# Kernel optimization log

Measured on AMD Instinct MI355X. Metric: run time of the kernel, lower is better.

The kernel has to match this reference:

```python
import jax, jax.numpy as jnp
import numpy as np

N, E, H, DE = 50000, 800000, 128, 16

def silu(x):
    return x * jax.nn.sigmoid(x)

def setup_inputs() -> dict:
    key = jax.random.key(0)
    ks = jax.random.split(key, 24)
    def W(k, i, o, s=0.02):
        return (jax.random.normal(k, (i, o), jnp.float32) * s)
    inp = {
        'h': jax.random.normal(ks[0], (N, H), jnp.float32),
        'coord': jax.random.normal(ks[1], (N, 3), jnp.float32),
        'edge_index': jax.random.randint(ks[2], (2, E), 0, N),
        'edge_attr': jax.random.normal(ks[3], (E, DE), jnp.float32),
        # mes_mlp: Linear(2H+1+DE -> H), SiLU, Linear(H -> H), SiLU
        'mes_w1': W(ks[4], 2 * H + 1 + DE, H), 'mes_b1': jnp.zeros((H,), jnp.float32),
        'mes_w2': W(ks[5], H, H),              'mes_b2': jnp.zeros((H,), jnp.float32),
        # edge_mlp: Linear(H+1+DE -> H), SiLU, Linear(H -> H)
        'edge_w1': W(ks[6], H + 1 + DE, H),    'edge_b1': jnp.zeros((H,), jnp.float32),
        'edge_w2': W(ks[7], H, H),             'edge_b2': jnp.zeros((H,), jnp.float32),
        # node_mlp: Linear(H+H -> H), SiLU, Linear(H -> H)
        'node_w1': W(ks[8], 2 * H, H),         'node_b1': jnp.zeros((H,), jnp.float32),
        'node_w2': W(ks[9], H, H),             'node_b2': jnp.zeros((H,), jnp.float32),
        # coord_mlp: Linear(H -> H), SiLU, Linear(H -> 1, no bias, xavier gain 0.001)
        'coord_w1': W(ks[10], H, H),           'coord_b1': jnp.zeros((H,), jnp.float32),
        'coord_w2': W(ks[11], H, 1, s=0.001),
    }
    return inp

def reference(h, coord, edge_index, edge_attr,
              mes_w1, mes_b1, mes_w2, mes_b2,
              edge_w1, edge_b1, edge_w2, edge_b2,
              node_w1, node_b1, node_w2, node_b2,
              coord_w1, coord_b1, coord_w2):
    row, col = edge_index[0], edge_index[1]
    n = h.shape[0]
    # coord2radial
    coord_diff = coord[row] - coord[col]                        # [E,3]
    radial = jnp.sum(coord_diff ** 2, axis=1, keepdims=True)    # [E,1]
    norm = jnp.sqrt(radial + 1e-8)
    coord_diff = coord_diff / (norm + 1.0)
    # mes_model
    mes_in = jnp.concatenate([h[row], h[col], radial, edge_attr], axis=1)
    edge_feat = silu(silu(mes_in @ mes_w1 + mes_b1) @ mes_w2 + mes_b2)  # [E,H]
    # coord_model (agg='sum', no tanh)
    trans = coord_diff * (silu(edge_feat @ coord_w1 + coord_b1) @ coord_w2)  # [E,3]
    coord = coord + jax.ops.segment_sum(trans, col, num_segments=n)
    # node_model (recurrent)
    agg = jax.ops.segment_sum(edge_feat, col, num_segments=n)   # [N,H]
    node_in = jnp.concatenate([h, agg], axis=1)
    h = h + (silu(node_in @ node_w1 + node_b1) @ node_w2 + node_b2)
    # edge_model
    edge_in = jnp.concatenate([edge_feat, radial, edge_attr], axis=1)
    edge_out = silu(edge_in @ edge_w1 + edge_b1) @ edge_w2 + edge_b2
    return (h, coord, edge_out)
```

## Files before the change

kernel.cpp:

```cpp
#include <hip/hip_runtime.h>
#include <cstdint>
#include <cstddef>

typedef float f32x4 __attribute__((ext_vector_type(4)));
typedef __bf16 bf16x8 __attribute__((ext_vector_type(8)));
typedef __bf16 bf16x4 __attribute__((ext_vector_type(4)));
typedef __bf16 bf16x2 __attribute__((ext_vector_type(2)));
typedef unsigned short u16;

#define Hdim 128
#define DEdim 16
#define TP 40

__device__ __forceinline__ float bf2f(uint32_t lo16){
  return __builtin_bit_cast(float, lo16 << 16);
}
__device__ __forceinline__ float bfhi(uint32_t v){
  return __builtin_bit_cast(float, v & 0xffff0000u);
}
__device__ __forceinline__ float silu_f(float x){
  return x / (1.0f + __expf(-x));
}
__device__ __forceinline__ uint32_t addbf2(uint32_t a, uint32_t b){
  float lo = bf2f(a & 0xffffu) + bf2f(b & 0xffffu);
  float hi = bfhi(a) + bfhi(b);
  bf16x2 p; p[0] = (__bf16)lo; p[1] = (__bf16)hi;
  return __builtin_bit_cast(uint32_t, p);
}
__device__ __forceinline__ uint2 pack4(f32x4 v){
  bf16x4 p;
  #pragma unroll
  for (int i=0;i<4;++i) p[i] = (__bf16)v[i];
  return __builtin_bit_cast(uint2, p);
}
__device__ __forceinline__ uint2 silu_pack4(const f32x4& v, f32x4* sout=nullptr){
  f32x4 s;
  #pragma unroll
  for (int i=0;i<4;++i) s[i] = silu_f(v[i]);
  if (sout) *sout = s;
  return pack4(s);
}

template<int KC>
__device__ __forceinline__ void gemm_sw(
    const u16* A, int apitch,
    const u16* __restrict__ Wt, int kpad, int woff,
    int wv, int cidx, int hi, f32x4 (&acc)[4][2])
{
  const u16* w0p = Wt + (size_t)((wv*2+0)*16 + cidx)*kpad + woff + hi*8;
  const u16* w1p = Wt + (size_t)((wv*2+1)*16 + cidx)*kpad + woff + hi*8;
  const u16* ap  = A + (size_t)cidx*apitch + hi*8;
  #pragma unroll
  for (int kc=0; kc<KC; ++kc){
    bf16x8 w0 = *(const bf16x8*)(w0p + kc*32);
    bf16x8 w1 = *(const bf16x8*)(w1p + kc*32);
    #pragma unroll
    for (int et=0; et<4; ++et){
      bf16x8 a = *(const bf16x8*)(ap + et*16*apitch + kc*32);
      acc[et][0] = __builtin_amdgcn_mfma_f32_16x16x32_bf16(w0, a, acc[et][0], 0,0,0);
      acc[et][1] = __builtin_amdgcn_mfma_f32_16x16x32_bf16(w1, a, acc[et][1], 0,0,0);
    }
  }
}

__device__ __forceinline__ void acc_bias(const float* __restrict__ bias,
                                         int wv, int hi, f32x4 (&acc)[4][2])
{
  f32x4 b0 = *(const f32x4*)(bias + (wv*2+0)*16 + hi*4);
  f32x4 b1 = *(const f32x4*)(bias + (wv*2+1)*16 + hi*4);
  #pragma unroll
  for (int et=0;et<4;++et){ acc[et][0]=b0; acc[et][1]=b1; }
}

template<int SP>
__device__ __forceinline__ void write_silu_S(u16* S, f32x4 (&acc)[4][2],
                                             int wv, int cidx, int hi)
{
  #pragma unroll
  for (int et=0; et<4; ++et){
    const int e = et*16 + cidx;
    #pragma unroll
    for (int j=0;j<2;++j){
      const int f0 = (wv*2+j)*16 + hi*4;
      *(uint2*)(S + (size_t)e*SP + f0) = silu_pack4(acc[et][j]);
    }
  }
}

template<bool PROJ, bool GATHER>
__global__ __launch_bounds__(256, PROJ?4:3) void egcl_edge(
    const float* __restrict__ h, const float* __restrict__ coord,
    const int* __restrict__ ei, const float* __restrict__ ea,
    const u16* __restrict__ proj, const int* __restrict__ pos,
    const float* __restrict__ mes_b1, const float* __restrict__ mes_b2,
    const float* __restrict__ edge_b1, const float* __restrict__ edge_b2,
    const float* __restrict__ coord_b1, const float* __restrict__ coord_w2,
    const u16* __restrict__ w_mes1t, const u16* __restrict__ w_mes2t,
    const u16* __restrict__ w_coord1t, const u16* __restrict__ w_edge1t,
    const u16* __restrict__ w_edge2t,
    float* __restrict__ agg, u16* __restrict__ featb,
    float* __restrict__ out_coord, float* __restrict__ out_edge, int E)
{
  constexpr int SP = PROJ ? 136 : 264;
  __shared__ u16 S[64*SP];
  __shared__ u16 T[64*TP];
  __shared__ float cds[64*4];
  __shared__ float tvs[4][64];
  __shared__ int cnode[64];
  __shared__ int epos[64];

  const int tid  = threadIdx.x;
  const int lane = tid & 63;
  const int wv   = tid >> 6;
  const int e0   = blockIdx.x * 64;
  const int cidx = lane & 15;
  const int hi   = lane >> 4;

  {
    const int le   = wv*16 + (lane>>2);
    const int part = lane & 3;
    int eg = e0 + le; if (eg >= E) eg = E-1;
    const int rn = ei[eg], cn = ei[E + eg];
    if constexpr (PROJ){
      const uint4* pr = (const uint4*)(proj + (size_t)rn*256 + part*32);
      const uint4* pc = (const uint4*)(proj + (size_t)cn*256 + 128 + part*32);
      u16* dst = S + (size_t)le*SP + part*32;
      #pragma unroll
      for (int q=0;q<4;++q){
        uint4 a = pr[q], b = pc[q], o;
        o.x = addbf2(a.x, b.x); o.y = addbf2(a.y, b.y);
        o.z = addbf2(a.z, b.z); o.w = addbf2(a.w, b.w);
        *(uint4*)(dst + q*8) = o;
      }
    } else {
      const float* src = ((part<2) ? h + (size_t)rn*Hdim : h + (size_t)cn*Hdim) + (part&1)*64;
      u16* dst = S + (size_t)le*SP + part*64;
      #pragma unroll
      for (int q=0;q<16;++q){
        float4 v = ((const float4*)src)[q];
        bf16x4 o = {(__bf16)v.x,(__bf16)v.y,(__bf16)v.z,(__bf16)v.w};
        *(bf16x4*)(dst + q*4) = o;
      }
    }
    if (part == 0){
      cnode[le] = cn;
      if constexpr (GATHER) epos[le] = pos[eg];
      const float dx = coord[(size_t)rn*3+0] - coord[(size_t)cn*3+0];
      const float dy = coord[(size_t)rn*3+1] - coord[(size_t)cn*3+1];
      const float dz = coord[(size_t)rn*3+2] - coord[(size_t)cn*3+2];
      const float radial = dx*dx + dy*dy + dz*dz;
      const float inv = 1.0f/(sqrtf(radial + 1e-8f) + 1.0f);
      cds[le*4+0]=dx*inv; cds[le*4+1]=dy*inv; cds[le*4+2]=dz*inv; cds[le*4+3]=radial;
      u16* tp = T + le*TP;
      const float4* eap = (const float4*)(ea + (size_t)eg*DEdim);
      #pragma unroll
      for (int q=0;q<4;++q){
        float4 v = eap[q];
        bf16x4 o = {(__bf16)v.x,(__bf16)v.y,(__bf16)v.z,(__bf16)v.w};
        *(bf16x4*)(tp + q*4) = o;
      }
      bf16x4 z = {(__bf16)0.f,(__bf16)0.f,(__bf16)0.f,(__bf16)0.f};
      *(bf16x4*)(tp+16) = z; *(bf16x4*)(tp+20) = z;
      *(bf16x4*)(tp+24) = z; *(bf16x4*)(tp+28) = z;
      *(__bf16*)(tp+16) = (__bf16)radial;
    }
    ((float*)tvs)[tid] = 0.f;
  }
  __syncthreads();

  f32x4 acc[4][2];

  acc_bias(mes_b1, wv, hi, acc);
  if constexpr (PROJ){
    #pragma unroll
    for (int et=0;et<4;++et){
      const int e = et*16 + cidx;
      #pragma unroll
      for (int j=0;j<2;++j){
        const int f0 = (wv*2+j)*16 + hi*4;
        ushort4 sv = *(const ushort4*)(S + (size_t)e*SP + f0);
        acc[et][j][0] += bf2f(sv.x); acc[et][j][1] += bf2f(sv.y);
        acc[et][j][2] += bf2f(sv.z); acc[et][j][3] += bf2f(sv.w);
      }
    }
    gemm_sw<1>(T, TP, w_mes1t, 288, 256, wv, cidx, hi, acc);
  } else {
    gemm_sw<8>(S, SP, w_mes1t, 288, 0,   wv, cidx, hi, acc);
    gemm_sw<1>(T, TP, w_mes1t, 288, 256, wv, cidx, hi, acc);
    __syncthreads();
  }
  write_silu_S<SP>(S, acc, wv, cidx, hi);
  __syncthreads();

  acc_bias(mes_b2, wv, hi, acc);
  gemm_sw<4>(S, SP, w_mes2t, 128, 0, wv, cidx, hi, acc);
  uint2 ps[4][2];
  #pragma unroll
  for (int et=0;et<4;++et)
    #pragma unroll
    for (int j=0;j<2;++j){
      f32x4 sv;
      ps[et][j] = silu_pack4(acc[et][j], &sv);
      if constexpr (!GATHER){
        const int e = et*16 + cidx;
        if (e0 + e < E){
          const int f0 = (wv*2+j)*16 + hi*4;
          #pragma unroll
          for (int i=0;i<4;++i)
            atomicAdd(agg + (size_t)cnode[e]*Hdim + f0 + i, sv[i]);
        }
      }
    }
  __syncthreads();
  #pragma unroll
  for (int et=0;et<4;++et)
    #pragma unroll
    for (int j=0;j<2;++j)
      *(uint2*)(S + (size_t)(et*16+cidx)*SP + (wv*2+j)*16 + hi*4) = ps[et][j];
  __syncthreads();

  if constexpr (GATHER){
    const int row = tid >> 2, seg = tid & 3;
    if (e0 + row < E){
      const int4* s = (const int4*)(S + (size_t)row*SP + seg*32);
      int4* d = (int4*)(featb + (size_t)epos[row]*Hdim + seg*32);
      d[0]=s[0]; d[1]=s[1]; d[2]=s[2]; d[3]=s[3];
    }
  }

  acc_bias(coord_b1, wv, hi, acc);
  gemm_sw<4>(S, SP, w_coord1t, 128, 0, wv, cidx, hi, acc);
  {
    f32x4 cw0 = *(const f32x4*)(coord_w2 + (wv*2+0)*16 + hi*4);
    f32x4 cw1 = *(const f32x4*)(coord_w2 + (wv*2+1)*16 + hi*4);
    #pragma unroll
    for (int et=0;et<4;++et){
      float p = 0.f;
      #pragma unroll
      for (int i=0;i<4;++i)
        p += silu_f(acc[et][0][i])*cw0[i] + silu_f(acc[et][1][i])*cw1[i];
      p += __shfl_xor(p, 16);
      p += __shfl_xor(p, 32);
      if (hi == 0) tvs[wv][et*16+cidx] = p;
    }
  }

  acc_bias(edge_b1, wv, hi, acc);
  gemm_sw<4>(S, SP, w_edge1t, 160, 0,   wv, cidx, hi, acc);
  gemm_sw<1>(T, TP, w_edge1t, 160, 128, wv, cidx, hi, acc);
  #pragma unroll
  for (int et=0;et<4;++et)
    #pragma unroll
    for (int j=0;j<2;++j)
      ps[et][j] = silu_pack4(acc[et][j]);
  __syncthreads();
  if (tid < 192){
    const int le = tid/3, d = tid - le*3;
    if (e0 + le < E){
      const float t4 = tvs[0][le]+tvs[1][le]+tvs[2][le]+tvs[3][le];
      atomicAdd(out_coord + (size_t)cnode[le]*3 + d, cds[le*4+d]*t4);
    }
  }
  #pragma unroll
  for (int et=0;et<4;++et)
    #pragma unroll
    for (int j=0;j<2;++j)
      *(uint2*)(S + (size_t)(et*16+cidx)*SP + (wv*2+j)*16 + hi*4) = ps[et][j];
  __syncthreads();

  acc_bias(edge_b2, wv, hi, acc);
  gemm_sw<4>(S, SP, w_edge2t, 128, 0, wv, cidx, hi, acc);
  #pragma unroll
  for (int et=0;et<4;++et){
    const int e = e0 + et*16 + cidx;
    if (e < E){
      #pragma unroll
      for (int j=0;j<2;++j)
        *(f32x4*)(out_edge + (size_t)e*Hdim + (wv*2+j)*16 + hi*4) = acc[et][j];
    }
  }
}

__global__ __launch_bounds__(256, 4) void egcl_proj(
    const float* __restrict__ h, const u16* __restrict__ w_mes1t,
    u16* __restrict__ proj, int N)
{
  __shared__ u16 S[64*136];
  const int tid=threadIdx.x, lane=tid&63, wv=tid>>6, cidx=lane&15, hi=lane>>4;
  const int r0 = blockIdx.x*64, half = blockIdx.y;
  {
    const int le = tid>>2, part = tid&3;
    int g = r0 + le; if (g >= N) g = N-1;
    const float* src = h + (size_t)g*Hdim + part*32;
    u16* dst = S + (size_t)le*136 + part*32;
    #pragma unroll
    for (int q=0;q<8;++q){
      float4 v = ((const float4*)src)[q];
      bf16x4 o = {(__bf16)v.x,(__bf16)v.y,(__bf16)v.z,(__bf16)v.w};
      *(bf16x4*)(dst + q*4) = o;
    }
  }
  __syncthreads();
  f32x4 acc[4][2];
  #pragma unroll
  for (int et=0;et<4;++et){ acc[et][0]=(f32x4){0,0,0,0}; acc[et][1]=(f32x4){0,0,0,0}; }
  gemm_sw<4>(S, 136, w_mes1t, 288, half*128, wv, cidx, hi, acc);
  #pragma unroll
  for (int et=0;et<4;++et){
    const int g = r0 + et*16 + cidx;
    if (g < N){
      #pragma unroll
      for (int j=0;j<2;++j)
        *(uint2*)(proj + (size_t)g*256 + half*128 + (wv*2+j)*16 + hi*4) = pack4(acc[et][j]);
    }
  }
}

template<bool GATHER>
__global__ __launch_bounds__(256, 4) void egcl_node(
    const float* __restrict__ h, const float* __restrict__ agg,
    const int* __restrict__ offs, const int* __restrict__ deg,
    const u16* __restrict__ featb,
    const float* __restrict__ node_b1, const float* __restrict__ node_b2,
    const u16* __restrict__ w_node1t, const u16* __restrict__ w_node2t,
    float* __restrict__ out_h, int N)
{
  __shared__ u16 Ab[64*264];
  const int tid=threadIdx.x, lane=tid&63, wv=tid>>6, cidx=lane&15, hi=lane>>4;
  const int r0 = blockIdx.x*64;
  {
    const int le = tid>>2, part = tid&3;
    int g = r0 + le; if (g >= N) g = N-1;
    const float* src = h + (size_t)g*Hdim + part*32;
    u16* dst = Ab + (size_t)le*264 + part*32;
    #pragma unroll
    for (int q=0;q<8;++q){
      float4 v = ((const float4*)src)[q];
      bf16x4 o = {(__bf16)v.x,(__bf16)v.y,(__bf16)v.z,(__bf16)v.w};
      *(bf16x4*)(dst + q*4) = o;
    }
  }
  if constexpr (GATHER){
    const int le = tid>>2, part = tid&3;
    const int g = r0 + le;
    float a[32];
    #pragma unroll
    for (int q=0;q<32;++q) a[q]=0.f;
    if (g < N){
      const int s = offs[g], dg = deg[g];
      const u16* base = featb + (size_t)s*Hdim + part*32;
      #pragma unroll 2
      for (int r=0;r<dg;++r){
        const uint4* rp = (const uint4*)(base + (size_t)r*Hdim);
        #pragma unroll
        for (int q=0;q<4;++q){
          uint4 w = rp[q];
          a[q*8+0] += bf2f(w.x & 0xffffu); a[q*8+1] += bfhi(w.x);
          a[q*8+2] += bf2f(w.y & 0xffffu); a[q*8+3] += bfhi(w.y);
          a[q*8+4] += bf2f(w.z & 0xffffu); a[q*8+5] += bfhi(w.z);
          a[q*8+6] += bf2f(w.w & 0xffffu); a[q*8+7] += bfhi(w.w);
        }
      }
    }
    u16* dst = Ab + (size_t)le*264 + 128 + part*32;
    #pragma unroll
    for (int q=0;q<8;++q){
      bf16x4 o = {(__bf16)a[q*4+0],(__bf16)a[q*4+1],(__bf16)a[q*4+2],(__bf16)a[q*4+3]};
      *(bf16x4*)(dst + q*4) = o;
    }
  } else {
    const int le = tid>>2, part = tid&3;
    int g = r0 + le; if (g >= N) g = N-1;
    const float* src = agg + (size_t)g*Hdim + part*32;
    u16* dst = Ab + (size_t)le*264 + 128 + part*32;
    #pragma unroll
    for (int q=0;q<8;++q){
      float4 v = ((const float4*)src)[q];
      bf16x4 o = {(__bf16)v.x,(__bf16)v.y,(__bf16)v.z,(__bf16)v.w};
      *(bf16x4*)(dst + q*4) = o;
    }
  }
  __syncthreads();

  f32x4 acc[4][2];
  acc_bias(node_b1, wv, hi, acc);
  gemm_sw<8>(Ab, 264, w_node1t, 256, 0, wv, cidx, hi, acc);
  __syncthreads();
  write_silu_S<264>(Ab, acc, wv, cidx, hi);
  __syncthreads();
  acc_bias(node_b2, wv, hi, acc);
  gemm_sw<4>(Ab, 264, w_node2t, 128, 0, wv, cidx, hi, acc);
  #pragma unroll
  for (int et=0;et<4;++et){
    const int g = r0 + et*16 + cidx;
    if (g < N){
      #pragma unroll
      for (int j=0;j<2;++j){
        const int f0 = (wv*2+j)*16 + hi*4;
        f32x4 hv = *(const f32x4*)(h + (size_t)g*Hdim + f0);
        hv += acc[et][j];
        *(f32x4*)(out_h + (size_t)g*Hdim + f0) = hv;
      }
    }
  }
}

__global__ void egcl_init(const float* __restrict__ coord, float* __restrict__ out_coord,
                          int nc, float* __restrict__ zf, int nzf,
                          int* __restrict__ zi, int nzi)
{
  const int i = blockIdx.x*256 + threadIdx.x;
  if (i < nc) out_coord[i] = coord[i];
  if (zf && i < nzf) zf[i] = 0.f;
  if (zi && i < nzi) zi[i] = 0;
}

__global__ void egcl_wconv7(
    const float* s0, const float* s1, const float* s2, const float* s3,
    const float* s4, const float* s5, const float* s6, u16* __restrict__ dst)
{
  static const int kpads[7]  = {288,128,128,160,128,256,128};
  static const int Ks[7]     = {273,128,128,145,128,256,128};
  static const int modes[7]  = {1,0,0,2,0,0,0};
  const int gi = blockIdx.x*256 + threadIdx.x;
  int w = 0, off = 0, boff = 0;
  #pragma unroll
  for (int t=0;t<7;++t){
    const int sz = 128*kpads[t];
    if (gi >= off && gi < off + sz){ w = t; boff = off; }
    off += sz;
  }
  if (gi >= off) return;
  const float* srcs[7] = {s0,s1,s2,s3,s4,s5,s6};
  const int li = gi - boff;
  const int kpad = kpads[w], K = Ks[w], mode = modes[w];
  const int c = li / kpad, k = li - c*kpad;
  int ks;
  if (mode==1)      ks = (k<256) ? k : (k<272 ? k+1 : (k==272 ? 256 : -1));
  else if (mode==2) ks = (k<128) ? k : (k<144 ? k+1 : (k==144 ? 128 : -1));
  else              ks = (k<K) ? k : -1;
  const float v = (ks>=0) ? srcs[w][(size_t)ks*128 + c] : 0.f;
  *(__bf16*)(dst + gi) = (__bf16)v;
}

__global__ void k_hist(const int* __restrict__ ei, int* __restrict__ hist, int E){
  const int i = blockIdx.x*256 + threadIdx.x;
  if (i < E) atomicAdd(&hist[ei[E + i]], 1);
}
__global__ void k_scan1(const int* __restrict__ hist, int* __restrict__ partial, int N){
  __shared__ int s[256];
  const int t = threadIdx.x, i = blockIdx.x*256 + t;
  s[t] = (i < N) ? hist[i] : 0;
  __syncthreads();
  for (int o=128; o>0; o>>=1){ if (t < o) s[t] += s[t+o]; __syncthreads(); }
  if (t == 0) partial[blockIdx.x] = s[0];
}
__global__ void k_scan2(int* __restrict__ partial, int G){
  if (blockIdx.x == 0 && threadIdx.x == 0){
    int run = 0;
    for (int i=0;i<G;++i){ const int v = partial[i]; partial[i] = run; run += v; }
  }
}
__global__ void k_scan3(const int* __restrict__ hist, const int* __restrict__ partial,
                        int* __restrict__ offs, int* __restrict__ cursor, int N){
  __shared__ int s[256];
  const int t = threadIdx.x, i = blockIdx.x*256 + t;
  const int v = (i < N) ? hist[i] : 0;
  s[t] = v;
  __syncthreads();
  for (int o=1; o<256; o<<=1){
    int x = (t >= o) ? s[t-o] : 0;
    __syncthreads();
    s[t] += x;
    __syncthreads();
  }
  const int ex = s[t] - v + partial[blockIdx.x];
  if (i < N){ offs[i] = ex; cursor[i] = ex; }
}
__global__ void k_scatter(const int* __restrict__ ei, int* __restrict__ cursor,
                          int* __restrict__ pos, int E){
  const int i = blockIdx.x*256 + threadIdx.x;
  if (i < E){
    const int c = ei[E + i];
    pos[i] = atomicAdd(&cursor[c], 1);
  }
}

extern "C" void kernel_launch(void* const* d_in, const int* in_sizes, int n_in,
                              void* d_out, int out_size, void* d_ws, size_t ws_size,
                              hipStream_t stream)
{
  const float* h       = (const float*)d_in[0];
  const float* coord   = (const float*)d_in[1];
  const int*   ei      = (const int*)d_in[2];
  const float* ea      = (const float*)d_in[3];
  const float* mes_w1  = (const float*)d_in[4];
  const float* mes_b1  = (const float*)d_in[5];
  const float* mes_w2  = (const float*)d_in[6];
  const float* mes_b2  = (const float*)d_in[7];
  const float* edge_w1 = (const float*)d_in[8];
  const float* edge_b1 = (const float*)d_in[9];
  const float* edge_w2 = (const float*)d_in[10];
  const float* edge_b2 = (const float*)d_in[11];
  const float* node_w1 = (const float*)d_in[12];
  const float* node_b1 = (const float*)d_in[13];
  const float* node_w2 = (const float*)d_in[14];
  const float* node_b2 = (const float*)d_in[15];
  const float* coord_w1= (const float*)d_in[16];
  const float* coord_b1= (const float*)d_in[17];
  const float* coord_w2= (const float*)d_in[18];

  const int N = in_sizes[0] / Hdim;
  const int E = in_sizes[2] / 2;
  const int G1 = (N + 255) / 256;

  char* ws = (char*)d_ws;
  const size_t wtot = (size_t)(288+128+128+160+128+256+128)*128;
  u16* wbase     = (u16*)ws;
  u16* w_mes1t   = wbase;
  u16* w_mes2t   = w_mes1t  + 128*288;
  u16* w_coord1t = w_mes2t  + 128*128;
  u16* w_edge1t  = w_coord1t+ 128*128;
  u16* w_edge2t  = w_edge1t + 128*160;
  u16* w_node1t  = w_edge2t + 128*128;
  u16* w_node2t  = w_node1t + 128*256;

  auto al = [](size_t x){ return (x + 255) & ~(size_t)255; };
  const size_t base   = al(wtot*2);
  const size_t o_feat = base;
  const size_t o_hist = o_feat + al((size_t)E*Hdim*2);
  const size_t o_offs = o_hist + al((size_t)N*4);
  const size_t o_cur  = o_offs + al((size_t)N*4);
  const size_t o_part = o_cur  + al((size_t)N*4);
  const size_t o_pos  = o_part + al((size_t)G1*4);
  const size_t gather_end = o_pos + al((size_t)E*4);
  const size_t o_proj = gather_end;
  const size_t proj_end = o_proj + (size_t)N*256*2;
  const bool gather = (ws_size >= gather_end);
  const bool proj   = (ws_size >= proj_end);

  float* out_h     = (float*)d_out;
  float* out_coord = out_h + (size_t)N*Hdim;
  float* out_edge  = out_coord + (size_t)N*3;

  const int wblocks = (int)((wtot + 255)/256);
  egcl_wconv7<<<wblocks, 256, 0, stream>>>(mes_w1, mes_w2, coord_w1, edge_w1,
                                           edge_w2, node_w1, node_w2, wbase);

  if (gather){
    u16* featb  = (u16*)(ws + o_feat);
    int* hist   = (int*)(ws + o_hist);
    int* offs   = (int*)(ws + o_offs);
    int* cursor = (int*)(ws + o_cur);
    int* partial= (int*)(ws + o_part);
    int* pos    = (int*)(ws + o_pos);
    u16* projp  = (u16*)(ws + o_proj);

    egcl_init<<<(N*3+255)/256, 256, 0, stream>>>(coord, out_coord, N*3, nullptr, 0, hist, N);
    k_hist<<<(E+255)/256, 256, 0, stream>>>(ei, hist, E);
    k_scan1<<<G1, 256, 0, stream>>>(hist, partial, N);
    k_scan2<<<1, 64, 0, stream>>>(partial, G1);
    k_scan3<<<G1, 256, 0, stream>>>(hist, partial, offs, cursor, N);
    k_scatter<<<(E+255)/256, 256, 0, stream>>>(ei, cursor, pos, E);

    if (proj){
      dim3 pg((N+63)/64, 2);
      egcl_proj<<<pg, 256, 0, stream>>>(h, w_mes1t, projp, N);
      egcl_edge<true,true><<<(E+63)/64, 256, 0, stream>>>(h, coord, ei, ea, projp, pos,
          mes_b1, mes_b2, edge_b1, edge_b2, coord_b1, coord_w2,
          w_mes1t, w_mes2t, w_coord1t, w_edge1t, w_edge2t,
          nullptr, featb, out_coord, out_edge, E);
    } else {
      egcl_edge<false,true><<<(E+63)/64, 256, 0, stream>>>(h, coord, ei, ea, nullptr, pos,
          mes_b1, mes_b2, edge_b1, edge_b2, coord_b1, coord_w2,
          w_mes1t, w_mes2t, w_coord1t, w_edge1t, w_edge2t,
          nullptr, featb, out_coord, out_edge, E);
    }
    egcl_node<true><<<(N+63)/64, 256, 0, stream>>>(h, nullptr, offs, hist, featb,
        node_b1, node_b2, w_node1t, w_node2t, out_h, N);
  } else {
    float* agg = (float*)(ws + base);
    egcl_init<<<(N*Hdim+255)/256, 256, 0, stream>>>(coord, out_coord, N*3, agg, N*Hdim, nullptr, 0);
    egcl_edge<false,false><<<(E+63)/64, 256, 0, stream>>>(h, coord, ei, ea, nullptr, nullptr,
        mes_b1, mes_b2, edge_b1, edge_b2, coord_b1, coord_w2,
        w_mes1t, w_mes2t, w_coord1t, w_edge1t, w_edge2t,
        agg, nullptr, out_coord, out_edge, E);
    egcl_node<false><<<(N+63)/64, 256, 0, stream>>>(h, agg, nullptr, nullptr, nullptr,
        node_b1, node_b2, w_node1t, w_node2t, out_h, N);
  }
}
```

Before: 636.8 us.

## Give each wave its own 16-edge slab and drop block-wide barriers

Work is repartitioned so that each wave owns 16 edges (or nodes) and computes all 128 output features for them, rather than all four waves sharing 64 edges split by feature. Every wave now reads and writes only its own slice of shared memory, so all __syncthreads calls and the cross-wave reduction through tvs are removed. Launch bounds for the non-projection path are also raised to 4 blocks. The cost is that each wave now reads the whole weight matrix from global or L1 for only 16 edges, so weight traffic per edge goes up fourfold, and the 8 accumulators plus the preloaded A fragments increase register pressure.

```diff
diff --git a/kernel.cpp b/kernel.cpp
--- a/kernel.cpp
+++ b/kernel.cpp
@@ -42,6 +42,38 @@
 }
 
 template<int KC>
+__device__ __forceinline__ void gemm_w(
+    const u16* Sw, int sp,
+    const u16* __restrict__ Wt, int kpad, int woff,
+    int cidx, int hi, f32x4 (&acc)[8])
+{
+  bf16x8 a[KC];
+  const u16* ap = Sw + (size_t)cidx*sp + hi*8;
+  #pragma unroll
+  for (int kc=0; kc<KC; ++kc) a[kc] = *(const bf16x8*)(ap + kc*32);
+  #pragma unroll
+  for (int j=0;j<8;++j){
+    const u16* wp = Wt + (size_t)(j*16+cidx)*kpad + woff + hi*8;
+    #pragma unroll
+    for (int kc=0; kc<KC; ++kc){
+      bf16x8 w = *(const bf16x8*)(wp + kc*32);
+      acc[j] = __builtin_amdgcn_mfma_f32_16x16x32_bf16(w, a[kc], acc[j], 0,0,0);
+    }
+  }
+}
+
+__device__ __forceinline__ void bias8(const float* __restrict__ b, int hi, f32x4 (&acc)[8]){
+  #pragma unroll
+  for (int j=0;j<8;++j) acc[j] = *(const f32x4*)(b + j*16 + hi*4);
+}
+
+__device__ __forceinline__ void silu_store8(u16* Sw, int sp, int cidx, int hi, f32x4 (&acc)[8]){
+  #pragma unroll
+  for (int j=0;j<8;++j)
+    *(uint2*)(Sw + (size_t)cidx*sp + j*16 + hi*4) = silu_pack4(acc[j]);
+}
+
+template<int KC>
 __device__ __forceinline__ void gemm_sw(
     const u16* A, int apitch,
     const u16* __restrict__ Wt, int kpad, int woff,
@@ -63,32 +95,8 @@
   }
 }
 
-__device__ __forceinline__ void acc_bias(const float* __restrict__ bias,
-                                         int wv, int hi, f32x4 (&acc)[4][2])
-{
-  f32x4 b0 = *(const f32x4*)(bias + (wv*2+0)*16 + hi*4);
-  f32x4 b1 = *(const f32x4*)(bias + (wv*2+1)*16 + hi*4);
-  #pragma unroll
-  for (int et=0;et<4;++et){ acc[et][0]=b0; acc[et][1]=b1; }
-}
-
-template<int SP>
-__device__ __forceinline__ void write_silu_S(u16* S, f32x4 (&acc)[4][2],
-                                             int wv, int cidx, int hi)
-{
-  #pragma unroll
-  for (int et=0; et<4; ++et){
-    const int e = et*16 + cidx;
-    #pragma unroll
-    for (int j=0;j<2;++j){
-      const int f0 = (wv*2+j)*16 + hi*4;
-      *(uint2*)(S + (size_t)e*SP + f0) = silu_pack4(acc[et][j]);
-    }
-  }
-}
-
 template<bool PROJ, bool GATHER>
-__global__ __launch_bounds__(256, PROJ?4:3) void egcl_edge(
+__global__ __launch_bounds__(256, 4) void egcl_edge(
     const float* __restrict__ h, const float* __restrict__ coord,
     const int* __restrict__ ei, const float* __restrict__ ea,
     const u16* __restrict__ proj, const int* __restrict__ pos,
@@ -105,26 +113,28 @@
   __shared__ u16 S[64*SP];
   __shared__ u16 T[64*TP];
   __shared__ float cds[64*4];
-  __shared__ float tvs[4][64];
+  __shared__ float tvs[64];
   __shared__ int cnode[64];
   __shared__ int epos[64];
 
   const int tid  = threadIdx.x;
   const int lane = tid & 63;
   const int wv   = tid >> 6;
-  const int e0   = blockIdx.x * 64;
   const int cidx = lane & 15;
   const int hi   = lane >> 4;
+  const int e0   = blockIdx.x*64 + wv*16;
+  u16* Sw = S + (size_t)wv*16*SP;
+  u16* Tw = T + (size_t)wv*16*TP;
 
   {
-    const int le   = wv*16 + (lane>>2);
+    const int le   = lane >> 2;
     const int part = lane & 3;
     int eg = e0 + le; if (eg >= E) eg = E-1;
     const int rn = ei[eg], cn = ei[E + eg];
     if constexpr (PROJ){
       const uint4* pr = (const uint4*)(proj + (size_t)rn*256 + part*32);
       const uint4* pc = (const uint4*)(proj + (size_t)cn*256 + 128 + part*32);
-      u16* dst = S + (size_t)le*SP + part*32;
+      u16* dst = Sw + (size_t)le*SP + part*32;
       #pragma unroll
       for (int q=0;q<4;++q){
         uint4 a = pr[q], b = pc[q], o;
@@ -134,7 +144,7 @@
       }
     } else {
       const float* src = ((part<2) ? h + (size_t)rn*Hdim : h + (size_t)cn*Hdim) + (part&1)*64;
-      u16* dst = S + (size_t)le*SP + part*64;
+      u16* dst = Sw + (size_t)le*SP + part*64;
       #pragma unroll
       for (int q=0;q<16;++q){
         float4 v = ((const float4*)src)[q];
@@ -143,15 +153,16 @@
       }
     }
     if (part == 0){
-      cnode[le] = cn;
-      if constexpr (GATHER) epos[le] = pos[eg];
+      const int gle = wv*16 + le;
+      cnode[gle] = cn;
+      if constexpr (GATHER) epos[gle] = pos[eg];
       const float dx = coord[(size_t)rn*3+0] - coord[(size_t)cn*3+0];
       const float dy = coord[(size_t)rn*3+1] - coord[(size_t)cn*3+1];
       const float dz = coord[(size_t)rn*3+2] - coord[(size_t)cn*3+2];
       const float radial = dx*dx + dy*dy + dz*dz;
       const float inv = 1.0f/(sqrtf(radial + 1e-8f) + 1.0f);
-      cds[le*4+0]=dx*inv; cds[le*4+1]=dy*inv; cds[le*4+2]=dz*inv; cds[le*4+3]=radial;
-      u16* tp = T + le*TP;
+      cds[gle*4+0]=dx*inv; cds[gle*4+1]=dy*inv; cds[gle*4+2]=dz*inv; cds[gle*4+3]=radial;
+      u16* tp = Tw + le*TP;
       const float4* eap = (const float4*)(ea + (size_t)eg*DEdim);
       #pragma unroll
       for (int q=0;q<4;++q){
@@ -164,119 +175,84 @@
       *(bf16x4*)(tp+24) = z; *(bf16x4*)(tp+28) = z;
       *(__bf16*)(tp+16) = (__bf16)radial;
     }
-    ((float*)tvs)[tid] = 0.f;
-  }
-  __syncthreads();
-
-  f32x4 acc[4][2];
-
-  acc_bias(mes_b1, wv, hi, acc);
+  }
+
+  f32x4 acc[8];
+
+  bias8(mes_b1, hi, acc);
   if constexpr (PROJ){
     #pragma unroll
-    for (int et=0;et<4;++et){
-      const int e = et*16 + cidx;
-      #pragma unroll
-      for (int j=0;j<2;++j){
-        const int f0 = (wv*2+j)*16 + hi*4;
-        ushort4 sv = *(const ushort4*)(S + (size_t)e*SP + f0);
-        acc[et][j][0] += bf2f(sv.x); acc[et][j][1] += bf2f(sv.y);
-        acc[et][j][2] += bf2f(sv.z); acc[et][j][3] += bf2f(sv.w);
+    for (int j=0;j<8;++j){
+      ushort4 sv = *(const ushort4*)(Sw + (size_t)cidx*SP + j*16 + hi*4);
+      acc[j][0] += bf2f(sv.x); acc[j][1] += bf2f(sv.y);
+      acc[j][2] += bf2f(sv.z); acc[j][3] += bf2f(sv.w);
+    }
+  } else {
+    gemm_w<4>(Sw,       SP, w_mes1t, 288, 0,   cidx, hi, acc);
+    gemm_w<4>(Sw + 128, SP, w_mes1t, 288, 128, cidx, hi, acc);
+  }
+  gemm_w<1>(Tw, TP, w_mes1t, 288, 256, cidx, hi, acc);
+  silu_store8(Sw, SP, cidx, hi, acc);
+
+  bias8(mes_b2, hi, acc);
+  gemm_w<4>(Sw, SP, w_mes2t, 128, 0, cidx, hi, acc);
+  #pragma unroll
+  for (int j=0;j<8;++j){
+    f32x4 sv;
+    uint2 pk = silu_pack4(acc[j], &sv);
+    *(uint2*)(Sw + (size_t)cidx*SP + j*16 + hi*4) = pk;
+    if constexpr (!GATHER){
+      if (e0 + cidx < E){
+        #pragma unroll
+        for (int i=0;i<4;++i)
+          atomicAdd(agg + (size_t)cnode[wv*16+cidx]*Hdim + j*16 + hi*4 + i, sv[i]);
       }
     }
-    gemm_sw<1>(T, TP, w_mes1t, 288, 256, wv, cidx, hi, acc);
-  } else {
-    gemm_sw<8>(S, SP, w_mes1t, 288, 0,   wv, cidx, hi, acc);
-    gemm_sw<1>(T, TP, w_mes1t, 288, 256, wv, cidx, hi, acc);
-    __syncthreads();
-  }
-  write_silu_S<SP>(S, acc, wv, cidx, hi);
-  __syncthreads();
-
-  acc_bias(mes_b2, wv, hi, acc);
-  gemm_sw<4>(S, SP, w_mes2t, 128, 0, wv, cidx, hi, acc);
-  uint2 ps[4][2];
-  #pragma unroll
-  for (int et=0;et<4;++et)
-    #pragma unroll
-    for (int j=0;j<2;++j){
-      f32x4 sv;
-      ps[et][j] = silu_pack4(acc[et][j], &sv);
-      if constexpr (!GATHER){
-        const int e = et*16 + cidx;
-        if (e0 + e < E){
-          const int f0 = (wv*2+j)*16 + hi*4;
-          #pragma unroll
-          for (int i=0;i<4;++i)
-            atomicAdd(agg + (size_t)cnode[e]*Hdim + f0 + i, sv[i]);
-        }
-      }
-    }
-  __syncthreads();
-  #pragma unroll
-  for (int et=0;et<4;++et)
-    #pragma unroll
-    for (int j=0;j<2;++j)
-      *(uint2*)(S + (size_t)(et*16+cidx)*SP + (wv*2+j)*16 + hi*4) = ps[et][j];
-  __syncthreads();
+  }
 
   if constexpr (GATHER){
-    const int row = tid >> 2, seg = tid & 3;
-    if (e0 + row < E){
-      const int4* s = (const int4*)(S + (size_t)row*SP + seg*32);
-      int4* d = (int4*)(featb + (size_t)epos[row]*Hdim + seg*32);
+    const int le = lane >> 2, seg = lane & 3;
+    if (e0 + le < E){
+      const int4* s = (const int4*)(Sw + (size_t)le*SP + seg*32);
+      int4* d = (int4*)(featb + (size_t)epos[wv*16+le]*Hdim + seg*32);
       d[0]=s[0]; d[1]=s[1]; d[2]=s[2]; d[3]=s[3];
     }
   }
 
-  acc_bias(coord_b1, wv, hi, acc);
-  gemm_sw<4>(S, SP, w_coord1t, 128, 0, wv, cidx, hi, acc);
+  bias8(coord_b1, hi, acc);
+  gemm_w<4>(Sw, SP, w_coord1t, 128, 0, cidx, hi, acc);
   {
-    f32x4 cw0 = *(const f32x4*)(coord_w2 + (wv*2+0)*16 + hi*4);
-    f32x4 cw1 = *(const f32x4*)(coord_w2 + (wv*2+1)*16 + hi*4);
-    #pragma unroll
-    for (int et=0;et<4;++et){
-      float p = 0.f;
-      #pragma unroll
-      for (int i=0;i<4;++i)
-        p += silu_f(acc[et][0][i])*cw0[i] + silu_f(acc[et][1][i])*cw1[i];
-      p += __shfl_xor(p, 16);
-      p += __shfl_xor(p, 32);
-      if (hi == 0) tvs[wv][et*16+cidx] = p;
-    }
-  }
-
-  acc_bias(edge_b1, wv, hi, acc);
-  gemm_sw<4>(S, SP, w_edge1t, 160, 0,   wv, cidx, hi, acc);
-  gemm_sw<1>(T, TP, w_edge1t, 160, 128, wv, cidx, hi, acc);
-  #pragma unroll
-  for (int et=0;et<4;++et)
-    #pragma unroll
-    for (int j=0;j<2;++j)
-      ps[et][j] = silu_pack4(acc[et][j]);
-  __syncthreads();
-  if (tid < 192){
-    const int le = tid/3, d = tid - le*3;
-    if (e0 + le < E){
-      const float t4 = tvs[0][le]+tvs[1][le]+tvs[2][le]+tvs[3][le];
-      atomicAdd(out_coord + (size_t)cnode[le]*3 + d, cds[le*4+d]*t4);
-    }
-  }
-  #pragma unroll
-  for (int et=0;et<4;++et)
-    #pragma unroll
-    for (int j=0;j<2;++j)
-      *(uint2*)(S + (size_t)(et*16+cidx)*SP + (wv*2+j)*16 + hi*4) = ps[et][j];
-  __syncthreads();
-
-  acc_bias(edge_b2, wv, hi, acc);
-  gemm_sw<4>(S, SP, w_edge2t, 128, 0, wv, cidx, hi, acc);
-  #pragma unroll
-  for (int et=0;et<4;++et){
-    const int e = e0 + et*16 + cidx;
+    float p = 0.f;
+    #pragma unroll
+    for (int j=0;j<8;++j){
+      f32x4 cw = *(const f32x4*)(coord_w2 + j*16 + hi*4);
+      #pragma unroll
+      for (int i=0;i<4;++i) p += silu_f(acc[j][i])*cw[i];
+    }
+    p += __shfl_xor(p, 16);
+    p += __shfl_xor(p, 32);
+    if (hi == 0) tvs[wv*16 + cidx] = p;
+  }
+  if (lane < 48){
+    const int le = lane/3, d = lane - le*3;
+    if (e0 + le < E)
+      atomicAdd(out_coord + (size_t)cnode[wv*16+le]*3 + d,
+                cds[(wv*16+le)*4+d]*tvs[wv*16+le]);
+  }
+
+  bias8(edge_b1, hi, acc);
+  gemm_w<4>(Sw, SP, w_edge1t, 160, 0,   cidx, hi, acc);
+  gemm_w<1>(Tw, TP, w_edge1t, 160, 128, cidx, hi, acc);
+  silu_store8(Sw, SP, cidx, hi, acc);
+
+  bias8(edge_b2, hi, acc);
+  gemm_w<4>(Sw, SP, w_edge2t, 128, 0, cidx, hi, acc);
+  {
+    const int e = e0 + cidx;
     if (e < E){
       #pragma unroll
-      for (int j=0;j<2;++j)
-        *(f32x4*)(out_edge + (size_t)e*Hdim + (wv*2+j)*16 + hi*4) = acc[et][j];
+      for (int j=0;j<8;++j)
+        *(f32x4*)(out_edge + (size_t)e*Hdim + j*16 + hi*4) = acc[j];
     }
   }
 }
@@ -327,12 +303,14 @@
 {
   __shared__ u16 Ab[64*264];
   const int tid=threadIdx.x, lane=tid&63, wv=tid>>6, cidx=lane&15, hi=lane>>4;
-  const int r0 = blockIdx.x*64;
+  const int r0 = blockIdx.x*64 + wv*16;
+  u16* Aw = Ab + (size_t)wv*16*264;
+
   {
-    const int le = tid>>2, part = tid&3;
+    const int le = lane>>2, part = lane&3;
     int g = r0 + le; if (g >= N) g = N-1;
     const float* src = h + (size_t)g*Hdim + part*32;
-    u16* dst = Ab + (size_t)le*264 + part*32;
+    u16* dst = Aw + (size_t)le*264 + part*32;
     #pragma unroll
     for (int q=0;q<8;++q){
       float4 v = ((const float4*)src)[q];
@@ -341,7 +319,7 @@
     }
   }
   if constexpr (GATHER){
-    const int le = tid>>2, part = tid&3;
+    const int le = lane>>2, part = lane&3;
     const int g = r0 + le;
     float a[32];
     #pragma unroll
@@ -362,17 +340,17 @@
         }
       }
     }
-    u16* dst = Ab + (size_t)le*264 + 128 + part*32;
+    u16* dst = Aw + (size_t)le*264 + 128 + part*32;
     #pragma unroll
     for (int q=0;q<8;++q){
       bf16x4 o = {(__bf16)a[q*4+0],(__bf16)a[q*4+1],(__bf16)a[q*4+2],(__bf16)a[q*4+3]};
       *(bf16x4*)(dst + q*4) = o;
     }
   } else {
-    const int le = tid>>2, part = tid&3;
+    const int le = lane>>2, part = lane&3;
     int g = r0 + le; if (g >= N) g = N-1;
     const float* src = agg + (size_t)g*Hdim + part*32;
-    u16* dst = Ab + (size_t)le*264 + 128 + part*32;
+    u16* dst = Aw + (size_t)le*264 + 128 + part*32;
     #pragma unroll
     for (int q=0;q<8;++q){
       float4 v = ((const float4*)src)[q];
@@ -380,25 +358,22 @@
       *(bf16x4*)(dst + q*4) = o;
     }
   }
-  __syncthreads();
-
-  f32x4 acc[4][2];
-  acc_bias(node_b1, wv, hi, acc);
-  gemm_sw<8>(Ab, 264, w_node1t, 256, 0, wv, cidx, hi, acc);
-  __syncthreads();
-  write_silu_S<264>(Ab, acc, wv, cidx, hi);
-  __syncthreads();
-  acc_bias(node_b2, wv, hi, acc);
-  gemm_sw<4>(Ab, 264, w_node2t, 128, 0, wv, cidx, hi, acc);
-  #pragma unroll
-  for (int et=0;et<4;++et){
-    const int g = r0 + et*16 + cidx;
+
+  f32x4 acc[8];
+  bias8(node_b1, hi, acc);
+  gemm_w<4>(Aw,       264, w_node1t, 256, 0,   cidx, hi, acc);
+  gemm_w<4>(Aw + 128, 264, w_node1t, 256, 128, cidx, hi, acc);
+  silu_store8(Aw, 264, cidx, hi, acc);
+  bias8(node_b2, hi, acc);
+  gemm_w<4>(Aw, 264, w_node2t, 128, 0, cidx, hi, acc);
+  {
+    const int g = r0 + cidx;
     if (g < N){
       #pragma unroll
-      for (int j=0;j<2;++j){
-        const int f0 = (wv*2+j)*16 + hi*4;
+      for (int j=0;j<8;++j){
+        const int f0 = j*16 + hi*4;
         f32x4 hv = *(const f32x4*)(h + (size_t)g*Hdim + f0);
-        hv += acc[et][j];
+        hv += acc[j];
         *(f32x4*)(out_h + (size_t)g*Hdim + f0) = hv;
       }
     }
```

After: 1.100 ms. +72.7%, slower.

## Store node projections in fp32 and gather them directly into accumulators

Applied to the files above, without the earlier changes.

The per-node first-layer projection is now stored in fp32 instead of bf16. Each lane gathers its own row and column projection slices straight into the MFMA accumulator registers, with no staging through shared memory and no bf16 add and unpack step. Divisions in silu and the coord normalisation are replaced with hardware reciprocal, and the tvs zeroing is dropped. In exchange the projection buffer doubles in size, so the gather moves twice the bytes per edge, and the larger workspace requirement may disable the proj path when the workspace is small.

```diff
diff --git a/kernel.cpp b/kernel.cpp
--- a/kernel.cpp
+++ b/kernel.cpp
@@ -5,7 +5,6 @@
 typedef float f32x4 __attribute__((ext_vector_type(4)));
 typedef __bf16 bf16x8 __attribute__((ext_vector_type(8)));
 typedef __bf16 bf16x4 __attribute__((ext_vector_type(4)));
-typedef __bf16 bf16x2 __attribute__((ext_vector_type(2)));
 typedef unsigned short u16;
 
 #define Hdim 128
@@ -19,13 +18,7 @@
   return __builtin_bit_cast(float, v & 0xffff0000u);
 }
 __device__ __forceinline__ float silu_f(float x){
-  return x / (1.0f + __expf(-x));
-}
-__device__ __forceinline__ uint32_t addbf2(uint32_t a, uint32_t b){
-  float lo = bf2f(a & 0xffffu) + bf2f(b & 0xffffu);
-  float hi = bfhi(a) + bfhi(b);
-  bf16x2 p; p[0] = (__bf16)lo; p[1] = (__bf16)hi;
-  return __builtin_bit_cast(uint32_t, p);
+  return x * __builtin_amdgcn_rcpf(1.0f + __expf(-x));
 }
 __device__ __forceinline__ uint2 pack4(f32x4 v){
   bf16x4 p;
@@ -91,7 +84,7 @@
 __global__ __launch_bounds__(256, PROJ?4:3) void egcl_edge(
     const float* __restrict__ h, const float* __restrict__ coord,
     const int* __restrict__ ei, const float* __restrict__ ea,
-    const u16* __restrict__ proj, const int* __restrict__ pos,
+    const float* __restrict__ projf, const int* __restrict__ pos,
     const float* __restrict__ mes_b1, const float* __restrict__ mes_b2,
     const float* __restrict__ edge_b1, const float* __restrict__ edge_b2,
     const float* __restrict__ coord_b1, const float* __restrict__ coord_w2,
@@ -116,23 +109,21 @@
   const int cidx = lane & 15;
   const int hi   = lane >> 4;
 
+  int rn4[4], cn4[4];
+  if constexpr (PROJ){
+    #pragma unroll
+    for (int et=0;et<4;++et){
+      int eg = e0 + et*16 + cidx; if (eg >= E) eg = E-1;
+      rn4[et] = ei[eg];  cn4[et] = ei[E + eg];
+    }
+  }
+
   {
     const int le   = wv*16 + (lane>>2);
     const int part = lane & 3;
     int eg = e0 + le; if (eg >= E) eg = E-1;
-    const int rn = ei[eg], cn = ei[E + eg];
-    if constexpr (PROJ){
-      const uint4* pr = (const uint4*)(proj + (size_t)rn*256 + part*32);
-      const uint4* pc = (const uint4*)(proj + (size_t)cn*256 + 128 + part*32);
-      u16* dst = S + (size_t)le*SP + part*32;
-      #pragma unroll
-      for (int q=0;q<4;++q){
-        uint4 a = pr[q], b = pc[q], o;
-        o.x = addbf2(a.x, b.x); o.y = addbf2(a.y, b.y);
-        o.z = addbf2(a.z, b.z); o.w = addbf2(a.w, b.w);
-        *(uint4*)(dst + q*8) = o;
-      }
-    } else {
+    if constexpr (!PROJ){
+      const int rn = ei[eg], cn = ei[E + eg];
       const float* src = ((part<2) ? h + (size_t)rn*Hdim : h + (size_t)cn*Hdim) + (part&1)*64;
       u16* dst = S + (size_t)le*SP + part*64;
       #pragma unroll
@@ -143,13 +134,14 @@
       }
     }
     if (part == 0){
+      const int rn = ei[eg], cn = ei[E + eg];
       cnode[le] = cn;
       if constexpr (GATHER) epos[le] = pos[eg];
       const float dx = coord[(size_t)rn*3+0] - coord[(size_t)cn*3+0];
       const float dy = coord[(size_t)rn*3+1] - coord[(size_t)cn*3+1];
       const float dz = coord[(size_t)rn*3+2] - coord[(size_t)cn*3+2];
       const float radial = dx*dx + dy*dy + dz*dz;
-      const float inv = 1.0f/(sqrtf(radial + 1e-8f) + 1.0f);
+      const float inv = __builtin_amdgcn_rcpf(sqrtf(radial + 1e-8f) + 1.0f);
       cds[le*4+0]=dx*inv; cds[le*4+1]=dy*inv; cds[le*4+2]=dz*inv; cds[le*4+3]=radial;
       u16* tp = T + le*TP;
       const float4* eap = (const float4*)(ea + (size_t)eg*DEdim);
@@ -164,7 +156,6 @@
       *(bf16x4*)(tp+24) = z; *(bf16x4*)(tp+28) = z;
       *(__bf16*)(tp+16) = (__bf16)radial;
     }
-    ((float*)tvs)[tid] = 0.f;
   }
   __syncthreads();
 
@@ -174,14 +165,15 @@
   if constexpr (PROJ){
     #pragma unroll
     for (int et=0;et<4;++et){
-      const int e = et*16 + cidx;
-      #pragma unroll
-      for (int j=0;j<2;++j){
-        const int f0 = (wv*2+j)*16 + hi*4;
-        ushort4 sv = *(const ushort4*)(S + (size_t)e*SP + f0);
-        acc[et][j][0] += bf2f(sv.x); acc[et][j][1] += bf2f(sv.y);
-        acc[et][j][2] += bf2f(sv.z); acc[et][j][3] += bf2f(sv.w);
-      }
+      const float* prow = projf + (size_t)rn4[et]*256 + wv*32 + hi*4;
+      acc[et][0] += *(const f32x4*)(prow);
+      acc[et][1] += *(const f32x4*)(prow + 16);
+    }
+    #pragma unroll
+    for (int et=0;et<4;++et){
+      const float* pcol = projf + (size_t)cn4[et]*256 + 128 + wv*32 + hi*4;
+      acc[et][0] += *(const f32x4*)(pcol);
+      acc[et][1] += *(const f32x4*)(pcol + 16);
     }
     gemm_sw<1>(T, TP, w_mes1t, 288, 256, wv, cidx, hi, acc);
   } else {
@@ -283,7 +275,7 @@
 
 __global__ __launch_bounds__(256, 4) void egcl_proj(
     const float* __restrict__ h, const u16* __restrict__ w_mes1t,
-    u16* __restrict__ proj, int N)
+    float* __restrict__ proj, int N)
 {
   __shared__ u16 S[64*136];
   const int tid=threadIdx.x, lane=tid&63, wv=tid>>6, cidx=lane&15, hi=lane>>4;
@@ -311,7 +303,7 @@
     if (g < N){
       #pragma unroll
       for (int j=0;j<2;++j)
-        *(uint2*)(proj + (size_t)g*256 + half*128 + (wv*2+j)*16 + hi*4) = pack4(acc[et][j]);
+        *(f32x4*)(proj + (size_t)g*256 + half*128 + (wv*2+j)*16 + hi*4) = acc[et][j];
     }
   }
 }
@@ -535,7 +527,7 @@
   const size_t o_pos  = o_part + al((size_t)G1*4);
   const size_t gather_end = o_pos + al((size_t)E*4);
   const size_t o_proj = gather_end;
-  const size_t proj_end = o_proj + (size_t)N*256*2;
+  const size_t proj_end = o_proj + (size_t)N*256*4;
   const bool gather = (ws_size >= gather_end);
   const bool proj   = (ws_size >= proj_end);
 
@@ -554,7 +546,7 @@
     int* cursor = (int*)(ws + o_cur);
     int* partial= (int*)(ws + o_part);
     int* pos    = (int*)(ws + o_pos);
-    u16* projp  = (u16*)(ws + o_proj);
+    float* projp= (float*)(ws + o_proj);
 
     egcl_init<<<(N*3+255)/256, 256, 0, stream>>>(coord, out_coord, N*3, nullptr, 0, hist, N);
     k_hist<<<(E+255)/256, 256, 0, stream>>>(ei, hist, E);
```

New measurement: 641.1 us. About the same (+0.7%).
